# Performance work log

Hardware: AMD Instinct MI355X
Metric: run time of the kernel (lower is better)

## Reference

```python
import jax, jax.numpy as jnp
import numpy as np

B, T, OBS = 16, 4095, 128
HID, NH, FF, NL = 256, 8, 1024, 4
DH = HID // NH
ACT = 32
KEPS = 0.001   # performer kernel_epsilon (generalized attention default)
LNEPS = 1e-6   # flax LayerNorm default eps


def setup_inputs() -> dict:
    key = jax.random.key(0)
    ks = list(jax.random.split(key, 16))
    s = 0.02
    r = lambda k, shape: jax.random.normal(k, shape, jnp.float32) * s
    return {
        "hidden_state": jnp.zeros((B, 1, HID), jnp.float32),
        "ins": jax.random.normal(ks[0], (B, T, OBS), jnp.float32),
        "resets": jax.random.randint(ks[1], (B,), 0, 2).astype(bool),
        "emb_W": r(ks[2], (OBS, HID)), "emb_b": jnp.zeros((HID,), jnp.float32),
        "Wq": r(ks[3], (NL, HID, NH, DH)), "bq": jnp.zeros((NL, NH, DH), jnp.float32),
        "Wk": r(ks[4], (NL, HID, NH, DH)), "bk": jnp.zeros((NL, NH, DH), jnp.float32),
        "Wv": r(ks[5], (NL, HID, NH, DH)), "bv": jnp.zeros((NL, NH, DH), jnp.float32),
        "Wo": r(ks[6], (NL, NH, DH, HID)), "bo": jnp.zeros((NL, HID), jnp.float32),
        "ln1_s": jnp.ones((NL, HID), jnp.float32), "ln1_b": jnp.zeros((NL, HID), jnp.float32),
        "W1": r(ks[7], (NL, HID, FF)), "b1": jnp.zeros((NL, FF), jnp.float32),
        "W2": r(ks[8], (NL, FF, HID)), "b2": jnp.zeros((NL, HID), jnp.float32),
        "ln2_s": jnp.ones((NL, HID), jnp.float32), "ln2_b": jnp.zeros((NL, HID), jnp.float32),
        "qp_W": r(ks[9], (HID, ACT)), "qp_b": jnp.zeros((ACT,), jnp.float32),
    }


def layer_norm(x, scale, bias):
    m = x.mean(-1, keepdims=True)
    v = ((x - m) ** 2).mean(-1, keepdims=True)
    return (x - m) * jax.lax.rsqrt(v + LNEPS) * scale + bias


def favor_attention(q, k, v):
    # FAVOR+ generalized attention with deterministic relu features (no random
    # projection, make_fast_generalized_attention defaults), bidirectional,
    # renormalized. q,k,v: [B, L, H, Dh]; feature dim M == Dh.
    qp = jax.nn.relu(q) + KEPS
    kp = jax.nn.relu(k) + KEPS
    kv = jnp.einsum('blhm,blhd->bhmd', kp, v)            # [B,H,M,Dh]
    num = jnp.einsum('blhm,bhmd->blhd', qp, kv)           # [B,L,H,Dh]
    den = jnp.einsum('blhm,bhm->blh', qp, kp.sum(axis=1))  # [B,L,H]
    return num / den[..., None]


def encoder_block(x, Wq, bq, Wk, bk, Wv, bv, Wo, bo, ln1_s, ln1_b, W1, b1, W2, b2, ln2_s, ln2_b):
    q = jnp.einsum('bld,dhm->blhm', x, Wq) + bq
    k = jnp.einsum('bld,dhm->blhm', x, Wk) + bk
    v = jnp.einsum('bld,dhm->blhm', x, Wv) + bv
    a = favor_attention(q, k, v)
    o = jnp.einsum('blhm,hmd->bld', a, Wo) + bo
    x = o + o  # faithful to source: x = attn(x); x = x + dropout(x)
    x = layer_norm(x, ln1_s, ln1_b)
    h = jax.nn.relu(x @ W1 + b1) @ W2 + b2
    h = h + h  # same residual quirk on the FFN branch
    return layer_norm(h, ln2_s, ln2_b)


def reference(hidden_state, ins, resets, emb_W, emb_b, Wq, bq, Wk, bk, Wv, bv, Wo, bo, ln1_s, ln1_b, W1, b1, W2, b2, ln2_s, ln2_b, qp_W, qp_b):
    emb = ins @ emb_W + emb_b                         # [B, T, HID]
    hs = jnp.where(resets[:, None, None], 0.0, hidden_state)
    x = jnp.concatenate([hs, emb], axis=-2)           # [B, 1+T, HID]
    for i in range(NL):
        x = encoder_block(x, Wq[i], bq[i], Wk[i], bk[i], Wv[i], bv[i], Wo[i], bo[i],
                          ln1_s[i], ln1_b[i], W1[i], b1[i], W2[i], b2[i], ln2_s[i], ln2_b[i])
    new_hidden = x[..., 0:1, :]                       # carry token
    q_vals = new_hidden @ qp_W + qp_b                 # [B, 1, ACT]
    return new_hidden, q_vals
```

## Files before the change

### kernel.cpp

```cpp
#include <hip/hip_runtime.h>


typedef unsigned short bf16_t;
typedef __attribute__((ext_vector_type(8))) short short8;
typedef __attribute__((ext_vector_type(4))) float float4v;

#define NB 16
#define LSEQ 4096
#define MROWS (NB * LSEQ)
#define HIDD 256
#define NHEAD 8
#define DHEAD 32
#define FFD 1024
#define NLAY 4
#define KEPS_F 1e-3f
#define LNEPS_F 1e-6f
#define KV_ELEMS (NB * NHEAD * 32 * 33)

__device__ __forceinline__ float b2f(bf16_t h) {
    return __uint_as_float(((unsigned int)h) << 16);
}
__device__ __forceinline__ bf16_t f2b(float f) {
    unsigned int u = __float_as_uint(f);
    u += 0x7fffu + ((u >> 16) & 1u);
    return (bf16_t)(u >> 16);
}

#define GLOAD_LDS16(g, l)                                                     \
    __builtin_amdgcn_global_load_lds(                                         \
        (const __attribute__((address_space(1))) void*)(g),                   \
        (__attribute__((address_space(3))) void*)(l), 16, 0, 0)

#define SBAR() __builtin_amdgcn_s_barrier()
#define WAITV(n)                                                              \
    do {                                                                      \
        asm volatile("s_waitcnt vmcnt(" #n ")" ::: "memory");                 \
        __builtin_amdgcn_sched_barrier(0);                                    \
    } while (0)

#define FRAG16(L, R)                                                          \
    (*(const short8*)&(L)[((((R) >> 1) * 8) +                                  \
        (((((R) & 1) << 2) | quad) ^ (((R) >> 1) & 7))) * 8])

__global__ __launch_bounds__(256) void conv_transpose_kernel(
    const float* __restrict__ in, bf16_t* __restrict__ out, int R, int C,
    size_t ils, size_t ols)
{
    __shared__ float tile[32][33];
    const size_t ib = (size_t)blockIdx.z * ils;
    const size_t ob = (size_t)blockIdx.z * ols;
    const int r0 = blockIdx.y * 32, c0 = blockIdx.x * 32;
    const int tx = threadIdx.x & 31, ty = threadIdx.x >> 5;
#pragma unroll
    for (int rr = ty; rr < 32; rr += 8)
        tile[rr][tx] = in[ib + (size_t)(r0 + rr) * C + c0 + tx];
    __syncthreads();
#pragma unroll
    for (int rr = ty; rr < 32; rr += 8)
        out[ob + (size_t)(c0 + rr) * R + r0 + tx] = f2b(tile[tx][rr]);
}

__global__ __launch_bounds__(256) void concat_bias_kernel(
    const float* __restrict__ bq, const float* __restrict__ bk,
    const float* __restrict__ bv, float* __restrict__ bqkv)
{
    const int l = blockIdx.x, j = threadIdx.x;
    bqkv[l * 768 + j]       = bq[l * 256 + j];
    bqkv[l * 768 + 256 + j] = bk[l * 256 + j];
    bqkv[l * 768 + 512 + j] = bv[l * 256 + j];
}

__global__ __launch_bounds__(256) void prep_a_kernel(
    const float* __restrict__ ins, bf16_t* __restrict__ Ain)
{
    const int row = blockIdx.x * 2 + (threadIdx.x >> 7);
    const int j = threadIdx.x & 127;
    const int b = row >> 12, l = row & (LSEQ - 1);
    bf16_t v = 0;
    if (l != 0) v = f2b(ins[((size_t)b * 4095 + (l - 1)) * 128 + j]);
    Ain[(size_t)row * 128 + j] = v;
}

__global__ __launch_bounds__(256) void fix_row0_kernel(
    const float* __restrict__ hidden, const int* __restrict__ resets,
    bf16_t* __restrict__ X)
{
    const int b = blockIdx.x, j = threadIdx.x;
    float v = resets[b] ? 0.f : hidden[b * HIDD + j];
    X[((size_t)b * LSEQ) * HIDD + j] = f2b(v);
}

template <int MODE>
__global__ __launch_bounds__(512, 4) void gemm_pipe(
    const bf16_t* __restrict__ A, const bf16_t* __restrict__ WT,
    const float* __restrict__ bias, bf16_t* __restrict__ C,
    int M, int N, int K, int lda, int ldc)
{
    __shared__ __align__(16) bf16_t As[3][128 * 32];
    __shared__ __align__(16) bf16_t Bs[3][256 * 32];

    const int tid = threadIdx.x;
    const int wave = tid >> 6, lane = tid & 63;
    const int quad = lane >> 4, mr = lane & 15;

    const int Nn = N >> 8;
    const int id = blockIdx.x;
    const int s = id >> 3;
    const int bm = (((id & 7) + ((s / Nn) << 3))) << 7;
    const int bn = (s % Nn) << 8;

    const int wm = (wave & 1) << 6;
    const int wn = (wave >> 1) << 6;

    const int KT = K >> 5;

    float bcol[4];
#pragma unroll
    for (int j = 0; j < 4; ++j) bcol[j] = bias[bn + wn + j * 16 + mr];
    asm volatile("s_waitcnt vmcnt(0)" ::: "memory");
    __builtin_amdgcn_sched_barrier(0);

    auto stageA = [&](int t) {
        const int k0 = t << 5;
        bf16_t* L = &As[t % 3][0];
        const int c = tid;
        const int r = c >> 2;
        const int up = ((((r & 1) << 2) | (c & 3)) ^ ((r >> 1) & 7));
        const int grow = ((r >> 1) << 1) | (up >> 2);
        GLOAD_LDS16(A + (size_t)(bm + grow) * lda + k0 + ((up & 3) << 3),
                    L + c * 8);
    };
    auto stageB = [&](int t) {
        const int k0 = t << 5;
        bf16_t* L = &Bs[t % 3][0];
#pragma unroll
        for (int it = 0; it < 2; ++it) {
            const int c = it * 512 + tid;
            const int r = c >> 2;
            const int up = ((((r & 1) << 2) | (c & 3)) ^ ((r >> 1) & 7));
            const int grow = ((r >> 1) << 1) | (up >> 2);
            GLOAD_LDS16(WT + (size_t)(bn + grow) * K + k0 + ((up & 3) << 3),
                        L + c * 8);
        }
    };

    float4v acc[4][4];
#pragma unroll
    for (int i = 0; i < 4; i++)
#pragma unroll
        for (int j = 0; j < 4; j++) acc[i][j] = (float4v)(0.f);

    const int P = KT < 2 ? KT : 2;
    for (int tt = 0; tt < P; ++tt) { stageA(tt); stageB(tt); }

    for (int t = 0; t < KT; ++t) {
        if (t < KT - 1) { WAITV(3); } else { WAITV(0); }
        SBAR();
        __builtin_amdgcn_sched_barrier(0);
        if (t + 2 < KT) { stageA(t + 2); stageB(t + 2); }
        const bf16_t* LA = &As[t % 3][0];
        const bf16_t* LB = &Bs[t % 3][0];
        short8 a[4], b[4];
#pragma unroll
        for (int j = 0; j < 4; ++j) b[j] = FRAG16(LB, wn + j * 16 + mr);
#pragma unroll
        for (int i = 0; i < 4; ++i) a[i] = FRAG16(LA, wm + i * 16 + mr);
        __builtin_amdgcn_s_setprio(1);
        __builtin_amdgcn_sched_barrier(0);
#pragma unroll
        for (int i = 0; i < 4; ++i)
#pragma unroll
            for (int j = 0; j < 4; ++j)
                acc[i][j] = __builtin_amdgcn_mfma_f32_16x16x32_bf16(
                    a[i], b[j], acc[i][j], 0, 0, 0);
        __builtin_amdgcn_sched_barrier(0);
        __builtin_amdgcn_s_setprio(0);
    }

#pragma unroll
    for (int i = 0; i < 4; ++i) {
#pragma unroll
        for (int r = 0; r < 4; ++r) {
            const int grow = bm + wm + i * 16 + quad * 4 + r;
            bf16_t* crow = C + (size_t)grow * ldc + bn + wn + mr;
#pragma unroll
            for (int j = 0; j < 4; ++j) {
                float v = acc[i][j][r] + bcol[j];
                if (MODE == 1) v = fmaxf(v, 0.f);
                crow[j * 16] = f2b(v);
            }
        }
    }
}

__global__ __launch_bounds__(512, 4) void gemm_ln_pipe(
    const bf16_t* __restrict__ A, const bf16_t* __restrict__ WT,
    const float* __restrict__ bias, const float* __restrict__ sc,
    const float* __restrict__ bi, bf16_t* __restrict__ out,
    int K, int lda)
{
    __shared__ __align__(16) bf16_t As[3][128 * 32];
    __shared__ __align__(16) bf16_t Bs[3][256 * 32];
    __shared__ float red[8][64][2];
    __shared__ float fin[128][2];

    const int tid = threadIdx.x;
    const int wave = tid >> 6, lane = tid & 63;
    const int quad = lane >> 4, mr = lane & 15;
    const int bm = blockIdx.x << 7;

    const int wm = (wave & 1) << 6;
    const int wn = (wave >> 1) << 6;

    const int KT = K >> 5;

    float bcol[4], scv[4], biv[4];
#pragma unroll
    for (int j = 0; j < 4; ++j) {
        bcol[j] = bias[wn + j * 16 + mr];
        scv[j]  = sc[wn + j * 16 + mr];
        biv[j]  = bi[wn + j * 16 + mr];
    }
    asm volatile("s_waitcnt vmcnt(0)" ::: "memory");
    __builtin_amdgcn_sched_barrier(0);

    auto stageA = [&](int t) {
        const int k0 = t << 5;
        bf16_t* L = &As[t % 3][0];
        const int c = tid;
        const int r = c >> 2;
        const int up = ((((r & 1) << 2) | (c & 3)) ^ ((r >> 1) & 7));
        const int grow = ((r >> 1) << 1) | (up >> 2);
        GLOAD_LDS16(A + (size_t)(bm + grow) * lda + k0 + ((up & 3) << 3),
                    L + c * 8);
    };
    auto stageB = [&](int t) {
        const int k0 = t << 5;
        bf16_t* L = &Bs[t % 3][0];
#pragma unroll
        for (int it = 0; it < 2; ++it) {
            const int c = it * 512 + tid;
            const int r = c >> 2;
            const int up = ((((r & 1) << 2) | (c & 3)) ^ ((r >> 1) & 7));
            const int grow = ((r >> 1) << 1) | (up >> 2);
            GLOAD_LDS16(WT + (size_t)grow * K + k0 + ((up & 3) << 3),
                        L + c * 8);
        }
    };

    float4v acc[4][4];
#pragma unroll
    for (int i = 0; i < 4; i++)
#pragma unroll
        for (int j = 0; j < 4; j++) acc[i][j] = (float4v)(0.f);

    const int P = KT < 2 ? KT : 2;
    for (int tt = 0; tt < P; ++tt) { stageA(tt); stageB(tt); }

    for (int t = 0; t < KT; ++t) {
        if (t < KT - 1) { WAITV(3); } else { WAITV(0); }
        SBAR();
        __builtin_amdgcn_sched_barrier(0);
        if (t + 2 < KT) { stageA(t + 2); stageB(t + 2); }
        const bf16_t* LA = &As[t % 3][0];
        const bf16_t* LB = &Bs[t % 3][0];
        short8 a[4], b[4];
#pragma unroll
        for (int j = 0; j < 4; ++j) b[j] = FRAG16(LB, wn + j * 16 + mr);
#pragma unroll
        for (int i = 0; i < 4; ++i) a[i] = FRAG16(LA, wm + i * 16 + mr);
        __builtin_amdgcn_s_setprio(1);
        __builtin_amdgcn_sched_barrier(0);
#pragma unroll
        for (int i = 0; i < 4; ++i)
#pragma unroll
            for (int j = 0; j < 4; ++j)
                acc[i][j] = __builtin_amdgcn_mfma_f32_16x16x32_bf16(
                    a[i], b[j], acc[i][j], 0, 0, 0);
        __builtin_amdgcn_sched_barrier(0);
        __builtin_amdgcn_s_setprio(0);
    }

#pragma unroll
    for (int i = 0; i < 4; ++i) {
#pragma unroll
        for (int r = 0; r < 4; ++r) {
            float ss = 0.f, s2 = 0.f;
#pragma unroll
            for (int j = 0; j < 4; ++j) {
                const float v = 2.0f * (acc[i][j][r] + bcol[j]);
                ss += v; s2 += v * v;
            }
#pragma unroll
            for (int off = 1; off < 16; off <<= 1) {
                ss += __shfl_xor(ss, off, 64);
                s2 += __shfl_xor(s2, off, 64);
            }
            if (mr == 0) {
                const int rl = i * 16 + quad * 4 + r;
                red[wave][rl][0] = ss;
                red[wave][rl][1] = s2;
            }
        }
    }
    __syncthreads();
    if (tid < 256) {
        const int R = tid >> 1, p = tid & 1;
        const int mh = R >> 6, rl = R & 63;
        fin[R][p] = red[mh][rl][p] + red[mh + 2][rl][p]
                  + red[mh + 4][rl][p] + red[mh + 6][rl][p];
    }
    __syncthreads();

#pragma unroll
    for (int i = 0; i < 4; ++i) {
#pragma unroll
        for (int r = 0; r < 4; ++r) {
            const int R = wm + i * 16 + quad * 4 + r;
            const float mean = fin[R][0] * (1.0f / 256.0f);
            const float var  = fin[R][1] * (1.0f / 256.0f) - mean * mean;
            const float rs = rsqrtf(var + LNEPS_F);
            bf16_t* crow = out + (size_t)(bm + R) * 256 + wn + mr;
#pragma unroll
            for (int j = 0; j < 4; ++j) {
                const float v = 2.0f * (acc[i][j][r] + bcol[j]);
                crow[j * 16] = f2b((v - mean) * rs * scv[j] + biv[j]);
            }
        }
    }
}

__global__ __launch_bounds__(512) void gemm_favor_ln_mfma(
    const bf16_t* __restrict__ QKV, const float* __restrict__ KV,
    const bf16_t* __restrict__ WT, const float* __restrict__ bias,
    const float* __restrict__ sc, const float* __restrict__ bi,
    bf16_t* __restrict__ out)
{
    __shared__ __align__(16) bf16_t As[128 * 64];
    __shared__ __align__(16) bf16_t Bs[256 * 64];
    __shared__ __align__(16) bf16_t kvT[NHEAD * 34 * 36];
    __shared__ float red[8][64][2];
    __shared__ float fin[128][2];

    const int tid = threadIdx.x;
    const int wave = tid >> 6, lane = tid & 63;
    const int bm = blockIdx.x * 128;
    const int b = bm >> 12;
    const int quad = lane >> 4, mr = lane & 15;
    const int mxor = mr & 7;
    const int wm0 = (wave & 1) * 64;
    const int wn0 = (wave >> 1) * 64;

    for (int e = tid; e < NHEAD * 34 * 32; e += 512) {
        const int h = e / (34 * 32);
        const int rem = e - h * (34 * 32);
        const int d = rem >> 5, m = rem & 31;
        bf16_t v = 0;
        if (d < 33) v = f2b(KV[((size_t)(b * NHEAD + h)) * (32 * 33) + m * 33 + d]);
        kvT[(h * 34 + d) * 36 + m] = v;
    }
    __syncthreads();

    float4v acc[4][4];
#pragma unroll
    for (int i = 0; i < 4; i++)
#pragma unroll
        for (int j = 0; j < 4; j++) acc[i][j] = (float4v)(0.f);

    for (int k0 = 0; k0 < 256; k0 += 64) {
#pragma unroll
        for (int it = 0; it < 4; it++) {
            const int c = it * 512 + tid;
            const int r = c >> 3;
            const int kofs = ((c & 7) ^ (r & 7)) * 8;
            GLOAD_LDS16(WT + (size_t)r * 256 + k0 + kofs, &Bs[c * 8]);
        }
        const int h0 = k0 >> 5;
        const int Rrow = bm + wave * 16 + mr;
#pragma unroll
        for (int hh = 0; hh < 2; hh++) {
            const int h = h0 + hh;
            short8 araw = *(const short8*)(QKV + (size_t)Rrow * 768 + h * 32 + quad * 8);
            short8 a;
#pragma unroll
            for (int j = 0; j < 8; j++)
                a[j] = (short)f2b(fmaxf(b2f((bf16_t)araw[j]), 0.f) + KEPS_F);
            short8 bf0 = *(const short8*)&kvT[(h * 34 + mr) * 36 + quad * 8];
            short8 bf1 = *(const short8*)&kvT[(h * 34 + 16 + mr) * 36 + quad * 8];
            short8 bden;
#pragma unroll
            for (int j = 0; j < 8; j++) bden[j] = 0;
            if (mr == 0)
                bden = *(const short8*)&kvT[(h * 34 + 32) * 36 + quad * 8];
            float4v c0 = __builtin_amdgcn_mfma_f32_16x16x32_bf16(a, bf0, (float4v)(0.f), 0, 0, 0);
            float4v c1 = __builtin_amdgcn_mfma_f32_16x16x32_bf16(a, bf1, (float4v)(0.f), 0, 0, 0);
            float4v c2 = __builtin_amdgcn_mfma_f32_16x16x32_bf16(a, bden, (float4v)(0.f), 0, 0, 0);
#pragma unroll
            for (int r = 0; r < 4; r++) {
                const float den = __shfl(c2[r], quad << 4);
                const float rinv = 1.0f / den;
                const int R = wave * 16 + quad * 4 + r;
                const int ca = hh * 32 + mr;
                const int cbn = hh * 32 + 16 + mr;
                As[(R * 8 + ((ca >> 3) ^ (R & 7))) * 8 + (ca & 7)]   = f2b(c0[r] * rinv);
                As[(R * 8 + ((cbn >> 3) ^ (R & 7))) * 8 + (cbn & 7)] = f2b(c1[r] * rinv);
            }
        }
        __syncthreads();
#pragma unroll
        for (int kk = 0; kk < 8; kk += 4) {
            short8 a[4], bfr[4];
#pragma unroll
            for (int i = 0; i < 4; i++)
                a[i] = *(const short8*)&As[((wm0 + i * 16 + mr) * 8 + ((quad + kk) ^ mxor)) * 8];
#pragma unroll
            for (int j = 0; j < 4; j++)
                bfr[j] = *(const short8*)&Bs[((wn0 + j * 16 + mr) * 8 + ((quad + kk) ^ mxor)) * 8];
#pragma unroll
            for (int i = 0; i < 4; i++)
#pragma unroll
                for (int j = 0; j < 4; j++)
                    acc[i][j] = __builtin_amdgcn_mfma_f32_16x16x32_bf16(
                        a[i], bfr[j], acc[i][j], 0, 0, 0);
        }
        __syncthreads();
    }

    float bcol[4];
#pragma unroll
    for (int j = 0; j < 4; j++) bcol[j] = bias[wn0 + j * 16 + mr];

#pragma unroll
    for (int i = 0; i < 4; i++) {
#pragma unroll
        for (int r = 0; r < 4; r++) {
            float s = 0.f, s2 = 0.f;
#pragma unroll
            for (int j = 0; j < 4; j++) {
                const float v = 2.0f * (acc[i][j][r] + bcol[j]);
                s += v; s2 += v * v;
            }
#pragma unroll
            for (int off = 1; off < 16; off <<= 1) {
                s  += __shfl_xor(s, off, 64);
                s2 += __shfl_xor(s2, off, 64);
            }
            if (mr == 0) {
                const int rl = i * 16 + quad * 4 + r;
                red[wave][rl][0] = s;
                red[wave][rl][1] = s2;
            }
        }
    }
    __syncthreads();
    if (tid < 256) {
        const int R = tid >> 1, p = tid & 1;
        const int mh = R >> 6, rl = R & 63;
        fin[R][p] = red[mh][rl][p] + red[mh + 2][rl][p]
                  + red[mh + 4][rl][p] + red[mh + 6][rl][p];
    }
    __syncthreads();

    float scv[4], biv[4];
#pragma unroll
    for (int j = 0; j < 4; j++) {
        scv[j] = sc[wn0 + j * 16 + mr];
        biv[j] = bi[wn0 + j * 16 + mr];
    }
#pragma unroll
    for (int i = 0; i < 4; i++) {
#pragma unroll
        for (int r = 0; r < 4; r++) {
            const int R = wm0 + i * 16 + quad * 4 + r;
            const float mean = fin[R][0] * (1.0f / 256.0f);
            const float var  = fin[R][1] * (1.0f / 256.0f) - mean * mean;
            const float rs = rsqrtf(var + LNEPS_F);
            bf16_t* crow = out + (size_t)(bm + R) * 256 + wn0 + mr;
#pragma unroll
            for (int j = 0; j < 4; j++) {
                const float v = 2.0f * (acc[i][j][r] + bcol[j]);
                crow[j * 16] = f2b((v - mean) * rs * scv[j] + biv[j]);
            }
        }
    }
}

__global__ __launch_bounds__(256) void zero_kv(float* __restrict__ KV)
{
    int i = blockIdx.x * 256 + threadIdx.x;
    if (i < KV_ELEMS) KV[i] = 0.f;
}

__global__ __launch_bounds__(256) void kv_mfma(
    const bf16_t* __restrict__ QKV, float* __restrict__ KV)
{
    __shared__ __align__(16) char smem[24576];
    bf16_t (*kp)[36] = (bf16_t(*)[36])smem;
    bf16_t (*vv)[52] = (bf16_t(*)[52])(smem + 9216);
    float (*red)[6][64][4] = (float(*)[6][64][4])smem;

    const int bh = blockIdx.x;
    const int b = bh >> 3, h = bh & 7;
    const size_t rowbase = (size_t)b * LSEQ + blockIdx.y * 512;
    const int tid = threadIdx.x;
    const int wave = tid >> 6, lane = tid & 63;
    const int quad = lane >> 4, mr = lane & 15;

    for (int e = tid; e < 128 * 20; e += 256) {
        const int l = e / 20, c = 32 + (e % 20);
        vv[l][c] = (c == 32) ? (bf16_t)0x3F80 : (bf16_t)0;
    }

    float4v acc[2][3];
#pragma unroll
    for (int i = 0; i < 2; i++)
#pragma unroll
        for (int t = 0; t < 3; t++) acc[i][t] = (float4v)(0.f);

    for (int pass = 0; pass < 4; pass++) {
        __syncthreads();
        const size_t lp = rowbase + pass * 128;
#pragma unroll
        for (int it = 0; it < 4; it++) {
            const int e = tid + it * 256;
            const int l = e >> 3, c0 = (e & 7) * 4;
            const bf16_t* src = QKV + (lp + l) * 768 + 256 + h * 32 + c0;
            ushort4 kq = *(const ushort4*)src;
            ushort4 vq = *(const ushort4*)(src + 256);
            ushort4 ko;
            ko.x = f2b(fmaxf(b2f(kq.x), 0.f) + KEPS_F);
            ko.y = f2b(fmaxf(b2f(kq.y), 0.f) + KEPS_F);
            ko.z = f2b(fmaxf(b2f(kq.z), 0.f) + KEPS_F);
            ko.w = f2b(fmaxf(b2f(kq.w), 0.f) + KEPS_F);
            *(ushort4*)&kp[l][c0] = ko;
            *(ushort4*)&vv[l][c0] = vq;
        }
        __syncthreads();

        const int lw = wave * 32 + quad * 8;
        short8 a[2], bb[3];
#pragma unroll
        for (int i = 0; i < 2; i++)
#pragma unroll
            for (int j = 0; j < 8; j++)
                a[i][j] = (short)kp[lw + j][i * 16 + mr];
#pragma unroll
        for (int t = 0; t < 3; t++)
#pragma unroll
            for (int j = 0; j < 8; j++)
                bb[t][j] = (short)vv[lw + j][t * 16 + mr];
#pragma unroll
        for (int i = 0; i < 2; i++)
#pragma unroll
            for (int t = 0; t < 3; t++)
                acc[i][t] = __builtin_amdgcn_mfma_f32_16x16x32_bf16(
                    a[i], bb[t], acc[i][t], 0, 0, 0);
    }

    __syncthreads();
#pragma unroll
    for (int i = 0; i < 2; i++)
#pragma unroll
        for (int t = 0; t < 3; t++)
#pragma unroll
            for (int r = 0; r < 4; r++)
                red[wave][i * 3 + t][lane][r] = acc[i][t][r];
    __syncthreads();

    float* dst = KV + (size_t)bh * (32 * 33);
    for (int e = tid; e < 6 * 64 * 4; e += 256) {
        const int t = e >> 8, li = (e >> 2) & 63, r = e & 3;
        const float s = red[0][t][li][r] + red[1][t][li][r]
                      + red[2][t][li][r] + red[3][t][li][r];
        const int i = t / 3, j = t % 3;
        const int m = i * 16 + (li >> 4) * 4 + r;
        const int d = j * 16 + (li & 15);
        if (d < 33) atomicAdd(&dst[m * 33 + d], s);
    }
}

__global__ __launch_bounds__(256) void head_kernel(
    const bf16_t* __restrict__ X, const float* __restrict__ qpW,
    const float* __restrict__ qpb, float* __restrict__ out)
{
    const int b = blockIdx.x, j = threadIdx.x;
    __shared__ float xr[HIDD];
    float v = b2f(X[((size_t)b * LSEQ) * HIDD + j]);
    xr[j] = v;
    out[b * HIDD + j] = v;
    __syncthreads();
    if (j < 32) {
        float acc = qpb[j];
        for (int d = 0; d < HIDD; d++)
            acc = fmaf(xr[d], qpW[d * 32 + j], acc);
        out[NB * HIDD + b * 32 + j] = acc;
    }
}

extern "C" void kernel_launch(void* const* d_in, const int* in_sizes, int n_in,
                              void* d_out, int out_size, void* d_ws, size_t ws_size,
                              hipStream_t stream)
{
    const float* hidden = (const float*)d_in[0];
    const float* ins    = (const float*)d_in[1];
    const int*   resets = (const int*)d_in[2];
    const float* embW   = (const float*)d_in[3];
    const float* embb   = (const float*)d_in[4];
    const float* Wq = (const float*)d_in[5];
    const float* bq = (const float*)d_in[6];
    const float* Wk = (const float*)d_in[7];
    const float* bk = (const float*)d_in[8];
    const float* Wv = (const float*)d_in[9];
    const float* bv = (const float*)d_in[10];
    const float* Wo = (const float*)d_in[11];
    const float* bo = (const float*)d_in[12];
    const float* ln1s = (const float*)d_in[13];
    const float* ln1b = (const float*)d_in[14];
    const float* W1 = (const float*)d_in[15];
    const float* b1 = (const float*)d_in[16];
    const float* W2 = (const float*)d_in[17];
    const float* b2 = (const float*)d_in[18];
    const float* ln2s = (const float*)d_in[19];
    const float* ln2b = (const float*)d_in[20];
    const float* qpW = (const float*)d_in[21];
    const float* qpb = (const float*)d_in[22];

    const size_t ACT_SZ = (size_t)MROWS * HIDD;
    bf16_t* X    = (bf16_t*)d_ws;
    bf16_t* QKV  = X + ACT_SZ;
    bf16_t* H1   = QKV;
    bf16_t* Ain  = QKV;
    float*  KV   = (float*)(QKV + (size_t)MROWS * FFD);
    float*  bqkv = KV + KV_ELEMS;
    bf16_t* WqkvT = (bf16_t*)(bqkv + NLAY * 768);
    bf16_t* WoT   = WqkvT + (size_t)NLAY * 3 * HIDD * HIDD;
    bf16_t* W1T   = WoT + (size_t)NLAY * HIDD * HIDD;
    bf16_t* W2T   = W1T + (size_t)NLAY * HIDD * FFD;
    bf16_t* embWT = W2T + (size_t)NLAY * FFD * HIDD;

    const dim3 blk(256);
    const dim3 blk512(512);
    const size_t HH = (size_t)HIDD * HIDD;

    conv_transpose_kernel<<<dim3(8, 8, NLAY), blk, 0, stream>>>(Wq, WqkvT,          HIDD, HIDD, HH, 3 * HH);
    conv_transpose_kernel<<<dim3(8, 8, NLAY), blk, 0, stream>>>(Wk, WqkvT + HH,     HIDD, HIDD, HH, 3 * HH);
    conv_transpose_kernel<<<dim3(8, 8, NLAY), blk, 0, stream>>>(Wv, WqkvT + 2 * HH, HIDD, HIDD, HH, 3 * HH);
    conv_transpose_kernel<<<dim3(8, 8, NLAY), blk, 0, stream>>>(Wo, WoT, HIDD, HIDD, HH, HH);
    conv_transpose_kernel<<<dim3(32, 8, NLAY), blk, 0, stream>>>(W1, W1T, HIDD, FFD, (size_t)HIDD * FFD, (size_t)HIDD * FFD);
    conv_transpose_kernel<<<dim3(8, 32, NLAY), blk, 0, stream>>>(W2, W2T, FFD, HIDD, (size_t)HIDD * FFD, (size_t)HIDD * FFD);
    conv_transpose_kernel<<<dim3(8, 4, 1), blk, 0, stream>>>(embW, embWT, 128, HIDD, 0, 0);
    concat_bias_kernel<<<NLAY, blk, 0, stream>>>(bq, bk, bv, bqkv);

    prep_a_kernel<<<MROWS / 2, blk, 0, stream>>>(ins, Ain);
    gemm_pipe<0><<<dim3(512), blk512, 0, stream>>>(Ain, embWT, embb, X, MROWS, HIDD, 128, 128, HIDD);
    fix_row0_kernel<<<NB, blk, 0, stream>>>(hidden, resets, X);

    for (int l = 0; l < NLAY; l++) {
        gemm_pipe<0><<<dim3(512 * 3), blk512, 0, stream>>>(X, WqkvT + (size_t)l * 3 * HH,
                                                           bqkv + l * 768, QKV, MROWS, 768, HIDD, HIDD, 768);

        zero_kv<<<(KV_ELEMS + 255) / 256, blk, 0, stream>>>(KV);
        kv_mfma<<<dim3(NB * NHEAD, 8), blk, 0, stream>>>(QKV, KV);

        gemm_favor_ln_mfma<<<MROWS / 128, blk512, 0, stream>>>(
            QKV, KV, WoT + (size_t)l * HH, bo + l * HIDD,
            ln1s + l * HIDD, ln1b + l * HIDD, X);

        gemm_pipe<1><<<dim3(512 * 4), blk512, 0, stream>>>(X, W1T + (size_t)l * HIDD * FFD,
                                                           b1 + l * FFD, H1, MROWS, FFD, HIDD, HIDD, FFD);
        gemm_ln_pipe<<<dim3(512), blk512, 0, stream>>>(
            H1, W2T + (size_t)l * FFD * HIDD, b2 + l * HIDD,
            ln2s + l * HIDD, ln2b + l * HIDD, X, FFD, FFD);
    }

    head_kernel<<<NB, blk, 0, stream>>>(X, qpW, qpb, (float*)d_out);
}
```

Baseline: 1.008 ms.

## Split FAVOR numerator computation from output projection GEMM with LayerNorm

Un-fuses the combined FAVOR-attention plus Wo GEMM plus LayerNorm kernel into two kernels. A standalone kernel computes the normalized attention output into a bf16 buffer, and the existing pipelined gemm_ln_pipe kernel then does the Wo projection with bias, the doubling residual and LayerNorm. This trades an extra activation round trip through global memory (32 MB written and read) for the better-pipelined GEMM in place of the serialized per-k-step compute inside the fused kernel.

```diff
diff --git a/kernel.cpp b/kernel.cpp
--- a/kernel.cpp
+++ b/kernel.cpp
@@ -330,26 +330,17 @@
     }
 }
 
-__global__ __launch_bounds__(512) void gemm_favor_ln_mfma(
+__global__ __launch_bounds__(512) void favor_a_kernel(
     const bf16_t* __restrict__ QKV, const float* __restrict__ KV,
-    const bf16_t* __restrict__ WT, const float* __restrict__ bias,
-    const float* __restrict__ sc, const float* __restrict__ bi,
-    bf16_t* __restrict__ out)
-{
-    __shared__ __align__(16) bf16_t As[128 * 64];
-    __shared__ __align__(16) bf16_t Bs[256 * 64];
+    bf16_t* __restrict__ Afav)
+{
     __shared__ __align__(16) bf16_t kvT[NHEAD * 34 * 36];
-    __shared__ float red[8][64][2];
-    __shared__ float fin[128][2];
 
     const int tid = threadIdx.x;
     const int wave = tid >> 6, lane = tid & 63;
     const int bm = blockIdx.x * 128;
     const int b = bm >> 12;
     const int quad = lane >> 4, mr = lane & 15;
-    const int mxor = mr & 7;
-    const int wm0 = (wave & 1) * 64;
-    const int wn0 = (wave >> 1) * 64;
 
     for (int e = tid; e < NHEAD * 34 * 32; e += 512) {
         const int h = e / (34 * 32);
@@ -361,126 +352,37 @@
     }
     __syncthreads();
 
-    float4v acc[4][4];
-#pragma unroll
-    for (int i = 0; i < 4; i++)
-#pragma unroll
-        for (int j = 0; j < 4; j++) acc[i][j] = (float4v)(0.f);
-
-    for (int k0 = 0; k0 < 256; k0 += 64) {
-#pragma unroll
-        for (int it = 0; it < 4; it++) {
-            const int c = it * 512 + tid;
-            const int r = c >> 3;
-            const int kofs = ((c & 7) ^ (r & 7)) * 8;
-            GLOAD_LDS16(WT + (size_t)r * 256 + k0 + kofs, &Bs[c * 8]);
-        }
-        const int h0 = k0 >> 5;
-        const int Rrow = bm + wave * 16 + mr;
-#pragma unroll
-        for (int hh = 0; hh < 2; hh++) {
-            const int h = h0 + hh;
-            short8 araw = *(const short8*)(QKV + (size_t)Rrow * 768 + h * 32 + quad * 8);
-            short8 a;
-#pragma unroll
-            for (int j = 0; j < 8; j++)
-                a[j] = (short)f2b(fmaxf(b2f((bf16_t)araw[j]), 0.f) + KEPS_F);
-            short8 bf0 = *(const short8*)&kvT[(h * 34 + mr) * 36 + quad * 8];
-            short8 bf1 = *(const short8*)&kvT[(h * 34 + 16 + mr) * 36 + quad * 8];
-            short8 bden;
-#pragma unroll
-            for (int j = 0; j < 8; j++) bden[j] = 0;
-            if (mr == 0)
-                bden = *(const short8*)&kvT[(h * 34 + 32) * 36 + quad * 8];
-            float4v c0 = __builtin_amdgcn_mfma_f32_16x16x32_bf16(a, bf0, (float4v)(0.f), 0, 0, 0);
-            float4v c1 = __builtin_amdgcn_mfma_f32_16x16x32_bf16(a, bf1, (float4v)(0.f), 0, 0, 0);
-            float4v c2 = __builtin_amdgcn_mfma_f32_16x16x32_bf16(a, bden, (float4v)(0.f), 0, 0, 0);
-#pragma unroll
-            for (int r = 0; r < 4; r++) {
-                const float den = __shfl(c2[r], quad << 4);
-                const float rinv = 1.0f / den;
-                const int R = wave * 16 + quad * 4 + r;
-                const int ca = hh * 32 + mr;
-                const int cbn = hh * 32 + 16 + mr;
-                As[(R * 8 + ((ca >> 3) ^ (R & 7))) * 8 + (ca & 7)]   = f2b(c0[r] * rinv);
-                As[(R * 8 + ((cbn >> 3) ^ (R & 7))) * 8 + (cbn & 7)] = f2b(c1[r] * rinv);
-            }
-        }
-        __syncthreads();
-#pragma unroll
-        for (int kk = 0; kk < 8; kk += 4) {
-            short8 a[4], bfr[4];
-#pragma unroll
-            for (int i = 0; i < 4; i++)
-                a[i] = *(const short8*)&As[((wm0 + i * 16 + mr) * 8 + ((quad + kk) ^ mxor)) * 8];
-#pragma unroll
-            for (int j = 0; j < 4; j++)
-                bfr[j] = *(const short8*)&Bs[((wn0 + j * 16 + mr) * 8 + ((quad + kk) ^ mxor)) * 8];
-#pragma unroll
-            for (int i = 0; i < 4; i++)
-#pragma unroll
-                for (int j = 0; j < 4; j++)
-                    acc[i][j] = __builtin_amdgcn_mfma_f32_16x16x32_bf16(
-                        a[i], bfr[j], acc[i][j], 0, 0, 0);
-        }
-        __syncthreads();
-    }
-
-    float bcol[4];
-#pragma unroll
-    for (int j = 0; j < 4; j++) bcol[j] = bias[wn0 + j * 16 + mr];
-
-#pragma unroll
-    for (int i = 0; i < 4; i++) {
+    const int Rrow = bm + wave * 16 + mr;
+    const size_t abase = (size_t)(bm + wave * 16) * 256;
+
+    short8 araw[NHEAD];
+#pragma unroll
+    for (int h = 0; h < NHEAD; ++h)
+        araw[h] = *(const short8*)(QKV + (size_t)Rrow * 768 + h * 32 + quad * 8);
+
+#pragma unroll
+    for (int h = 0; h < NHEAD; ++h) {
+        short8 a;
+#pragma unroll
+        for (int j = 0; j < 8; j++)
+            a[j] = (short)f2b(fmaxf(b2f((bf16_t)araw[h][j]), 0.f) + KEPS_F);
+        short8 bf0 = *(const short8*)&kvT[(h * 34 + mr) * 36 + quad * 8];
+        short8 bf1 = *(const short8*)&kvT[(h * 34 + 16 + mr) * 36 + quad * 8];
+        short8 bden;
+#pragma unroll
+        for (int j = 0; j < 8; j++) bden[j] = 0;
+        if (mr == 0)
+            bden = *(const short8*)&kvT[(h * 34 + 32) * 36 + quad * 8];
+        float4v c0 = __builtin_amdgcn_mfma_f32_16x16x32_bf16(a, bf0, (float4v)(0.f), 0, 0, 0);
+        float4v c1 = __builtin_amdgcn_mfma_f32_16x16x32_bf16(a, bf1, (float4v)(0.f), 0, 0, 0);
+        float4v c2 = __builtin_amdgcn_mfma_f32_16x16x32_bf16(a, bden, (float4v)(0.f), 0, 0, 0);
 #pragma unroll
         for (int r = 0; r < 4; r++) {
-            float s = 0.f, s2 = 0.f;
-#pragma unroll
-            for (int j = 0; j < 4; j++) {
-                const float v = 2.0f * (acc[i][j][r] + bcol[j]);
-                s += v; s2 += v * v;
-            }
-#pragma unroll
-            for (int off = 1; off < 16; off <<= 1) {
-                s  += __shfl_xor(s, off, 64);
-                s2 += __shfl_xor(s2, off, 64);
-            }
-            if (mr == 0) {
-                const int rl = i * 16 + quad * 4 + r;
-                red[wave][rl][0] = s;
-                red[wave][rl][1] = s2;
-            }
-        }
-    }
-    __syncthreads();
-    if (tid < 256) {
-        const int R = tid >> 1, p = tid & 1;
-        const int mh = R >> 6, rl = R & 63;
-        fin[R][p] = red[mh][rl][p] + red[mh + 2][rl][p]
-                  + red[mh + 4][rl][p] + red[mh + 6][rl][p];
-    }
-    __syncthreads();
-
-    float scv[4], biv[4];
-#pragma unroll
-    for (int j = 0; j < 4; j++) {
-        scv[j] = sc[wn0 + j * 16 + mr];
-        biv[j] = bi[wn0 + j * 16 + mr];
-    }
-#pragma unroll
-    for (int i = 0; i < 4; i++) {
-#pragma unroll
-        for (int r = 0; r < 4; r++) {
-            const int R = wm0 + i * 16 + quad * 4 + r;
-            const float mean = fin[R][0] * (1.0f / 256.0f);
-            const float var  = fin[R][1] * (1.0f / 256.0f) - mean * mean;
-            const float rs = rsqrtf(var + LNEPS_F);
-            bf16_t* crow = out + (size_t)(bm + R) * 256 + wn0 + mr;
-#pragma unroll
-            for (int j = 0; j < 4; j++) {
-                const float v = 2.0f * (acc[i][j][r] + bcol[j]);
-                crow[j * 16] = f2b((v - mean) * rs * scv[j] + biv[j]);
-            }
+            const float den = __shfl(c2[r], quad << 4);
+            const float rinv = 1.0f / den;
+            const int rl = quad * 4 + r;
+            Afav[abase + (size_t)rl * 256 + h * 32 + mr]      = f2b(c0[r] * rinv);
+            Afav[abase + (size_t)rl * 256 + h * 32 + 16 + mr] = f2b(c1[r] * rinv);
         }
     }
 }
@@ -630,6 +532,7 @@
     bf16_t* QKV  = X + ACT_SZ;
     bf16_t* H1   = QKV;
     bf16_t* Ain  = QKV;
+    bf16_t* Afav = QKV + (size_t)MROWS * 768;
     float*  KV   = (float*)(QKV + (size_t)MROWS * FFD);
     float*  bqkv = KV + KV_ELEMS;
     bf16_t* WqkvT = (bf16_t*)(bqkv + NLAY * 768);
@@ -662,9 +565,11 @@
         zero_kv<<<(KV_ELEMS + 255) / 256, blk, 0, stream>>>(KV);
         kv_mfma<<<dim3(NB * NHEAD, 8), blk, 0, stream>>>(QKV, KV);
 
-        gemm_favor_ln_mfma<<<MROWS / 128, blk512, 0, stream>>>(
-            QKV, KV, WoT + (size_t)l * HH, bo + l * HIDD,
-            ln1s + l * HIDD, ln1b + l * HIDD, X);
+        favor_a_kernel<<<dim3(MROWS / 128), blk512, 0, stream>>>(QKV, KV, Afav);
+
+        gemm_ln_pipe<<<dim3(512), blk512, 0, stream>>>(
+            Afav, WoT + (size_t)l * HH, bo + l * HIDD,
+            ln1s + l * HIDD, ln1b + l * HIDD, X, HIDD, HIDD);
 
         gemm_pipe<1><<<dim3(512 * 4), blk512, 0, stream>>>(X, W1T + (size_t)l * HIDD * FFD,
                                                            b1 + l * FFD, H1, MROWS, FFD, HIDD, HIDD, FFD);
```

After: 1.016 ms. Within noise of the previous version (+0.8%).
